# Kernel tuning notes

Hardware: AMD Instinct MI355X
Metric: run time of the kernel (lower is better)

## Reference

```python
import jax, jax.numpy as jnp
import numpy as np

B, C, H, W, E, HEADS = 8, 128, 96, 96, 16, 4
HD = C // HEADS

def _ln(x, g, b, eps=1e-5):
    m = jnp.mean(x, axis=-1, keepdims=True)
    v = jnp.mean(jnp.square(x - m), axis=-1, keepdims=True)
    return (x - m) * jax.lax.rsqrt(v + eps) * g + b

def _gelu(x):
    return jax.nn.gelu(x, approximate=False)  # torch nn.GELU default (erf)

def setup_inputs() -> dict:
    key = jax.random.key(0)
    ks = iter(jax.random.split(key, 48))
    def wgt(shape, s=0.02):
        return jax.random.normal(next(ks), shape, jnp.float32) * s
    d = {
        "feature_map": jax.random.normal(next(ks), (B, C, H, W), jnp.float32),
        "hyperedge_scores": jax.random.uniform(next(ks), (B, H * W, E), jnp.float32),
        # norm_node_pre
        "np_g": jnp.ones((C,), jnp.float32), "np_b": jnp.zeros((C,), jnp.float32),
        # MultiheadAttention (self-attn over hyperedges)
        "mha_w_in": wgt((3 * C, C)), "mha_b_in": jnp.zeros((3 * C,), jnp.float32),
        "mha_w_out": wgt((C, C)), "mha_b_out": jnp.zeros((C,), jnp.float32),
        # transformer FFN
        "ffn_w1": wgt((2 * C, C)), "ffn_b1": jnp.zeros((2 * C,), jnp.float32),
        "ffn_w2": wgt((C, 2 * C)), "ffn_b2": jnp.zeros((C,), jnp.float32),
        # shared LayerNorm inside HypergraphTransformerConv (used twice)
        "tnorm_g": jnp.ones((C,), jnp.float32), "tnorm_b": jnp.zeros((C,), jnp.float32),
        # norm_hyper
        "nh_g": jnp.ones((C,), jnp.float32), "nh_b": jnp.zeros((C,), jnp.float32),
        # hyper_proj
        "hp_w": wgt((C, C)), "hp_b": jnp.zeros((C,), jnp.float32),
        # HyperedgeGuidedNodeAttention
        "q_w": wgt((C, C)), "q_b": jnp.zeros((C,), jnp.float32),
        "kv_w": wgt((2 * C, C)), "kv_b": jnp.zeros((2 * C,), jnp.float32),
        # norm_fusion
        "nf_g": jnp.ones((2 * C,), jnp.float32), "nf_b": jnp.zeros((2 * C,), jnp.float32),
        # gate = Linear(2C->C) + LayerNorm(C) + Sigmoid
        "gate_w": wgt((C, 2 * C)), "gate_b": jnp.zeros((C,), jnp.float32),
        "gate_ln_g": jnp.ones((C,), jnp.float32), "gate_ln_b": jnp.zeros((C,), jnp.float32),
        # node_proj
        "nproj_w": wgt((C, C)), "nproj_b": jnp.zeros((C,), jnp.float32),
    }
    return d

def _forward(feature_map, hyperedge_scores, np_g, np_b, mha_w_in, mha_b_in,
             mha_w_out, mha_b_out, ffn_w1, ffn_b1, ffn_w2, ffn_b2,
             tnorm_g, tnorm_b, nh_g, nh_b, hp_w, hp_b, q_w, q_b, kv_w, kv_b,
             nf_g, nf_b, gate_w, gate_b, gate_ln_g, gate_ln_b, nproj_w, nproj_b):
    b, c, h, w = feature_map.shape
    n = h * w
    node = jnp.transpose(feature_map.reshape(b, c, n), (0, 2, 1))   # [B,N,C]
    node = _ln(node, np_g, np_b)
    # hyperedge aggregation: H^T @ X -> [B,E,C]
    hyper = jnp.einsum('bne,bnc->bec', hyperedge_scores, node)
    # --- HypergraphTransformerConv (self-attn over E=16 hyperedges) ---
    qkv = hyper @ mha_w_in.T + mha_b_in                               # [B,E,3C]
    q, k, v = jnp.split(qkv, 3, axis=-1)
    def heads(x):  # [B,E,C] -> [B,h,E,hd]
        return jnp.transpose(x.reshape(b, E, HEADS, HD), (0, 2, 1, 3))
    q, k, v = heads(q), heads(k), heads(v)
    attn = jax.nn.softmax(jnp.einsum('bhqd,bhkd->bhqk', q, k) / np.sqrt(HD), axis=-1)
    ao = jnp.einsum('bhqk,bhkd->bhqd', attn, v)
    ao = jnp.transpose(ao, (0, 2, 1, 3)).reshape(b, E, c)
    ao = ao @ mha_w_out.T + mha_b_out
    x = _ln(hyper + ao, tnorm_g, tnorm_b)
    ffn = _gelu(x @ ffn_w1.T + ffn_b1) @ ffn_w2.T + ffn_b2
    hyper = _ln(x + ffn, tnorm_g, tnorm_b)
    # ---
    hyper = _ln(hyper, nh_g, nh_b)
    hyper = _gelu(hyper @ hp_w.T + hp_b)                              # [B,E,C]
    intra = jnp.einsum('bne,bec->bnc', hyperedge_scores, hyper)       # [B,N,C]
    # HyperedgeGuidedNodeAttention (scale = C**-0.5)
    Q = node @ q_w.T + q_b
    K, V = jnp.split(hyper @ kv_w.T + kv_b, 2, axis=-1)
    a = jax.nn.softmax(jnp.einsum('bnc,bec->bne', Q, K) * (c ** -0.5), axis=-1)
    cross = jnp.einsum('bne,bec->bnc', a, V)
    combined = _ln(jnp.concatenate([intra, cross], axis=-1), nf_g, nf_b)
    gate = jax.nn.sigmoid(_ln(combined @ gate_w.T + gate_b, gate_ln_g, gate_ln_b))
    fused = gate * intra + (1.0 - gate) * cross
    upd = node + fused                                                # dropout in eval mode
    out = _gelu(upd @ nproj_w.T + nproj_b)
    return jnp.transpose(out, (0, 2, 1)).reshape(b, c, h, w)

def reference(feature_map, hyperedge_scores, np_g, np_b, mha_w_in, mha_b_in,
              mha_w_out, mha_b_out, ffn_w1, ffn_b1, ffn_w2, ffn_b2,
              tnorm_g, tnorm_b, nh_g, nh_b, hp_w, hp_b, q_w, q_b, kv_w, kv_b,
              nf_g, nf_b, gate_w, gate_b, gate_ln_g, gate_ln_b, nproj_w, nproj_b):
    return _forward(feature_map, hyperedge_scores, np_g, np_b, mha_w_in, mha_b_in,
                    mha_w_out, mha_b_out, ffn_w1, ffn_b1, ffn_w2, ffn_b2,
                    tnorm_g, tnorm_b, nh_g, nh_b, hp_w, hp_b, q_w, q_b, kv_w, kv_b,
                    nf_g, nf_b, gate_w, gate_b, gate_ln_g, gate_ln_b, nproj_w, nproj_b)
```

## Files before the change

kernel.cpp:

```cpp
#include <hip/hip_runtime.h>

typedef unsigned short bf_t;
typedef unsigned int u32;
typedef short short8 __attribute__((ext_vector_type(8)));
typedef float f32x4 __attribute__((ext_vector_type(4)));

#define NB 8
#define CC 128
#define NN 9216
#define EE 16

__device__ __forceinline__ float b2f(bf_t u){ return __uint_as_float(((u32)u)<<16); }
__device__ __forceinline__ bf_t f2b(float f){
  u32 u = __float_as_uint(f);
  u = (u + 0x7fffu + ((u>>16)&1u)) >> 16;
  return (bf_t)u;
}
__device__ __forceinline__ u32 pk2(float a, float b){
  return (u32)f2b(a) | ((u32)f2b(b)<<16);
}
__device__ __forceinline__ float gelu_f(float x){ return 0.5f*x*(1.f+erff(x*0.70710678118654752f)); }
__device__ __forceinline__ float red16(float v){
  #pragma unroll
  for (int m=1;m<16;m<<=1) v += __shfl_xor(v, m, 16);
  return v;
}
__device__ __forceinline__ float grs(float var){
  return rsqrtf(fmaxf(var + 1e-5f, 1e-8f));
}
__device__ __forceinline__ short8 ldw8(const float* __restrict__ p){
  float4 a = *(const float4*)p;
  float4 b = *(const float4*)(p+4);
  short8 o;
  o[0]=(short)f2b(a.x); o[1]=(short)f2b(a.y); o[2]=(short)f2b(a.z); o[3]=(short)f2b(a.w);
  o[4]=(short)f2b(b.x); o[5]=(short)f2b(b.y); o[6]=(short)f2b(b.z); o[7]=(short)f2b(b.w);
  return o;
}

__global__ __launch_bounds__(256) void k_zero(float* p){
  int i = blockIdx.x*256 + threadIdx.x;
  if (i < NB*EE*CC) p[i] = 0.f;
}

__global__ __launch_bounds__(256) void k_cvtw(const float* __restrict__ gw,
                                              const float* __restrict__ npw,
                                              bf_t* __restrict__ gwb,
                                              bf_t* __restrict__ npwb){
  int i = blockIdx.x*256 + threadIdx.x;
  gwb[i]        = f2b(gw[i]);
  gwb[i+16384]  = f2b(gw[i+16384]);
  npwb[i]       = f2b(npw[i]);
}

__global__ __launch_bounds__(256) void k_ln_agg(const float* __restrict__ fm,
                                                const float* __restrict__ g,
                                                const float* __restrict__ bb,
                                                const float* __restrict__ sc,
                                                float* __restrict__ nln,
                                                float* __restrict__ hacc){
  int b = blockIdx.y, tid = threadIdx.x;
  __shared__ float xs[128*65];
  __shared__ float scs[64][17];
  __shared__ float ps[4][64], pq[4][64], mrs[2][64];
  int cp = tid&63, eh = tid>>6;
  float a0[4]={0,0,0,0}, a1[4]={0,0,0,0};
  for (int ts=0; ts<4; ts++){
    int n0 = (blockIdx.x*4 + ts)*64;
    const float* base = fm + (size_t)b*CC*NN + n0;
    #pragma unroll
    for (int p=0;p<8;p++){
      int idx = tid + p*256;
      int c = idx>>4, n4 = (idx&15)*4;
      float4 v = *(const float4*)(base + (size_t)c*NN + n4);
      xs[c*65 + n4+0] = v.x; xs[c*65 + n4+1] = v.y;
      xs[c*65 + n4+2] = v.z; xs[c*65 + n4+3] = v.w;
    }
    { int n = tid>>2, e4 = (tid&3)*4;
      float4 sv = *(const float4*)(sc + ((size_t)(b*NN + n0 + n))*EE + e4);
      scs[n][e4+0] = sv.x; scs[n][e4+1] = sv.y;
      scs[n][e4+2] = sv.z; scs[n][e4+3] = sv.w;
    }
    __syncthreads();
    { int cg = tid>>6, n = tid&63;
      float s=0.f, q=0.f;
      #pragma unroll
      for (int c=0;c<32;c++){ float v = xs[(cg*32+c)*65 + n]; s+=v; q+=v*v; }
      ps[cg][n]=s; pq[cg][n]=q;
    }
    __syncthreads();
    if (tid < 64){
      float S = ps[0][tid]+ps[1][tid]+ps[2][tid]+ps[3][tid];
      float Q = pq[0][tid]+pq[1][tid]+pq[2][tid]+pq[3][tid];
      float m = S*(1.f/128.f);
      mrs[0][tid] = m; mrs[1][tid] = grs(Q*(1.f/128.f) - m*m);
    }
    __syncthreads();
    #pragma unroll
    for (int p=0;p<8;p++){
      int idx = tid + p*256;
      int c = idx>>4, n4 = (idx&15)*4;
      float gv = g[c], bv = bb[c];
      float4 o;
      float v0 = (xs[c*65+n4+0]-mrs[0][n4+0])*mrs[1][n4+0]*gv + bv;
      float v1 = (xs[c*65+n4+1]-mrs[0][n4+1])*mrs[1][n4+1]*gv + bv;
      float v2 = (xs[c*65+n4+2]-mrs[0][n4+2])*mrs[1][n4+2]*gv + bv;
      float v3 = (xs[c*65+n4+3]-mrs[0][n4+3])*mrs[1][n4+3]*gv + bv;
      o.x=v0; o.y=v1; o.z=v2; o.w=v3;
      xs[c*65+n4+0]=v0; xs[c*65+n4+1]=v1; xs[c*65+n4+2]=v2; xs[c*65+n4+3]=v3;
      *(float4*)(nln + ((size_t)(b*CC + c))*NN + n0 + n4) = o;
    }
    __syncthreads();
    for (int n=0;n<64;n++){
      float x0 = xs[cp*65 + n], x1 = xs[(cp+64)*65 + n];
      #pragma unroll
      for (int j=0;j<4;j++){
        float se = scs[n][eh*4+j];
        a0[j] += se*x0; a1[j] += se*x1;
      }
    }
    __syncthreads();
  }
  #pragma unroll
  for (int j=0;j<4;j++){
    float* hb = hacc + (size_t)(b*EE + eh*4 + j)*CC;
    atomicAdd(hb + cp, a0[j]);
    atomicAdd(hb + cp + 64, a1[j]);
  }
}

__device__ __forceinline__ void gemm16(const bf_t* A, int SA,
                                       const float* __restrict__ W,
                                       const float* __restrict__ bias,
                                       bf_t* O, int SO, int Nout, int K,
                                       int act, int tid){
  int lane = tid&63, wid = tid>>6;
  int m16 = lane&15, quad = lane>>4;
  for (int n0 = wid*16; n0 < Nout; n0 += 64){
    f32x4 acc = {0.f,0.f,0.f,0.f};
    for (int k0=0;k0<K;k0+=32){
      short8 af = *(const short8*)(A + m16*SA + k0 + quad*8);
      short8 bfv = ldw8(W + (size_t)(n0+m16)*K + k0 + quad*8);
      acc = __builtin_amdgcn_mfma_f32_16x16x32_bf16(af, bfv, acc, 0, 0, 0);
    }
    int col = n0 + m16;
    float bv = bias[col];
    #pragma unroll
    for (int r=0;r<4;r++){
      float v = acc[r] + bv;
      if (act) v = gelu_f(v);
      O[(quad*4+r)*SO + col] = f2b(v);
    }
  }
}

#define SP1 136
#define SP2 264
#define SP3 392

__global__ __launch_bounds__(256) void k_edge(const float* __restrict__ hacc,
    const float* w_in, const float* b_in, const float* w_out, const float* b_out,
    const float* w1, const float* b1, const float* w2, const float* b2v,
    const float* tg, const float* tb, const float* nhg, const float* nhb,
    const float* hpw, const float* hpb, const float* kvw, const float* kvbias,
    const float* qw, const float* qb,
    bf_t* __restrict__ hfw, bf_t* __restrict__ vws,
    float* __restrict__ Ktg, float* __restrict__ qbK){
  __shared__ __align__(16) bf_t hyp0[16*SP1];
  __shared__ __align__(16) bf_t qkvb[16*SP3];
  __shared__ __align__(16) bf_t aob [16*SP1];
  __shared__ __align__(16) bf_t xnb [16*SP1];
  __shared__ __align__(16) bf_t h1b [16*SP2];
  __shared__ __align__(16) bf_t t2b [16*SP1];
  __shared__ __align__(16) bf_t hfb [16*SP1];
  __shared__ __align__(16) bf_t kvo [16*SP2];
  int b = blockIdx.x, tid = threadIdx.x;

  #pragma unroll
  for (int p=0;p<8;p++){
    int idx = tid + p*256;
    int e = idx>>7, c = idx&127;
    hyp0[e*SP1 + c] = f2b(hacc[(size_t)(b*EE + e)*CC + c]);
  }
  __syncthreads();
  gemm16(hyp0, SP1, w_in, b_in, qkvb, SP3, 384, 128, 0, tid);
  __syncthreads();
  {
    int part = tid&3, hq = tid>>2;
    int h = hq>>4, qi = hq&15;
    int dbase = h*32 + part*8;
    float qv[8];
    #pragma unroll
    for (int j=0;j<8;j++) qv[j] = b2f(qkvb[qi*SP3 + dbase + j]);
    float dot[16];
    #pragma unroll
    for (int kk=0;kk<16;kk++){
      float s = 0.f;
      #pragma unroll
      for (int j=0;j<8;j++) s += qv[j]*b2f(qkvb[kk*SP3 + 128 + dbase + j]);
      dot[kk] = s;
    }
    #pragma unroll
    for (int m=1;m<4;m<<=1){
      #pragma unroll
      for (int kk=0;kk<16;kk++) dot[kk] += __shfl_xor(dot[kk], m, 4);
    }
    const float sc1 = 0.17677669529663687f;
    float mx = -1e30f;
    #pragma unroll
    for (int kk=0;kk<16;kk++){ dot[kk] *= sc1; mx = fmaxf(mx, dot[kk]); }
    float sum = 0.f;
    #pragma unroll
    for (int kk=0;kk<16;kk++){ dot[kk] = __expf(dot[kk]-mx); sum += dot[kk]; }
    float inv = 1.f/sum;
    float ao[8] = {0,0,0,0,0,0,0,0};
    #pragma unroll
    for (int kk=0;kk<16;kk++){
      float p = dot[kk]*inv;
      #pragma unroll
      for (int j=0;j<8;j++) ao[j] += p*b2f(qkvb[kk*SP3 + 256 + dbase + j]);
    }
    #pragma unroll
    for (int j=0;j<8;j++) aob[qi*SP1 + dbase + j] = f2b(ao[j]);
  }
  __syncthreads();
  gemm16(aob, SP1, w_out, b_out, xnb, SP1, 128, 128, 0, tid);
  __syncthreads();
  {
    int e = tid>>4, i = tid&15;
    float v[8]; float s=0.f, q=0.f;
    #pragma unroll
    for (int j=0;j<8;j++){
      int c = i*8+j;
      v[j] = b2f(hyp0[e*SP1+c]) + b2f(xnb[e*SP1+c]);
      s += v[j]; q += v[j]*v[j];
    }
    s = red16(s); q = red16(q);
    float m = s*(1.f/128.f);
    float rs = grs(q*(1.f/128.f) - m*m);
    #pragma unroll
    for (int j=0;j<8;j++){
      int c = i*8+j;
      xnb[e*SP1+c] = f2b((v[j]-m)*rs*tg[c] + tb[c]);
    }
  }
  __syncthreads();
  gemm16(xnb, SP1, w1, b1, h1b, SP2, 256, 128, 1, tid);
  __syncthreads();
  gemm16(h1b, SP2, w2, b2v, aob, SP1, 128, 256, 0, tid);
  __syncthreads();
  {
    int e = tid>>4, i = tid&15;
    float v[8]; float s=0.f, q=0.f;
    #pragma unroll
    for (int j=0;j<8;j++){
      int c = i*8+j;
      v[j] = b2f(xnb[e*SP1+c]) + b2f(aob[e*SP1+c]);
      s += v[j]; q += v[j]*v[j];
    }
    s = red16(s); q = red16(q);
    float m = s*(1.f/128.f);
    float rs = grs(q*(1.f/128.f) - m*m);
    float s2=0.f, q2=0.f;
    #pragma unroll
    for (int j=0;j<8;j++){
      int c = i*8+j;
      v[j] = (v[j]-m)*rs*tg[c] + tb[c];
      s2 += v[j]; q2 += v[j]*v[j];
    }
    s2 = red16(s2); q2 = red16(q2);
    float m2 = s2*(1.f/128.f);
    float rs2 = grs(q2*(1.f/128.f) - m2*m2);
    #pragma unroll
    for (int j=0;j<8;j++){
      int c = i*8+j;
      t2b[e*SP1+c] = f2b((v[j]-m2)*rs2*nhg[c] + nhb[c]);
    }
  }
  __syncthreads();
  gemm16(t2b, SP1, hpw, hpb, hfb, SP1, 128, 128, 1, tid);
  __syncthreads();
  gemm16(hfb, SP1, kvw, kvbias, kvo, SP2, 256, 128, 0, tid);
  __syncthreads();
  #pragma unroll
  for (int p=0;p<8;p++){
    int idx = tid + p*256;
    int e = idx>>7, c = idx&127;
    size_t o = (size_t)(b*EE + e)*CC + c;
    hfw[o] = hfb[e*SP1 + c];
    vws[o] = kvo[e*SP2 + 128 + c];
  }
  #pragma unroll
  for (int p=0;p<8;p++){
    int idx = tid + p*256;
    int e = idx>>7, c = idx&127;
    float s = 0.f;
    for (int d=0; d<128; d++) s += b2f(kvo[e*SP2 + d]) * qw[d*128 + c];
    Ktg[(size_t)(b*EE + e)*CC + c] = s;
  }
  if (tid < 16){
    float s = 0.f;
    for (int d=0; d<128; d++) s += qb[d] * b2f(kvo[tid*SP2 + d]);
    qbK[b*EE + tid] = s;
  }
}

template<int PRE>
__global__ __launch_bounds__(256) void k_meganode(
    float* __restrict__ io, const float* __restrict__ sc,
    const bf_t* __restrict__ hf, const bf_t* __restrict__ vw,
    const float* __restrict__ Ktg, const float* __restrict__ qbK,
    const float* __restrict__ nfg, const float* __restrict__ nfb,
    const float* __restrict__ gw, const bf_t* __restrict__ gwb,
    const float* __restrict__ gb,
    const float* __restrict__ glng, const float* __restrict__ glnb,
    const float* __restrict__ npw, const bf_t* __restrict__ npwb,
    const float* __restrict__ npb){
  int tid = threadIdx.x, lane = tid&63, wid = tid>>6;
  int m16 = lane&15, quad = lane>>4;
  int b = blockIdx.y, n0 = blockIdx.x*64;
  __shared__ __align__(16) bf_t xt[64*136];
  __shared__ __align__(16) char ctbuf[34816];
  __shared__ __align__(16) bf_t ktT[16*136];
  __shared__ __align__(16) bf_t hfT[128*24];
  __shared__ __align__(16) bf_t vfT[128*24];
  __shared__ __align__(16) bf_t a_sh[64*24];
  __shared__ float prm[1040];
  bf_t* ct = (bf_t*)ctbuf;
  float* ot = (float*)ctbuf;
  const short8 z8 = {0,0,0,0,0,0,0,0};

  #pragma unroll
  for (int p=0;p<8;p++){
    int idx = tid + p*256;
    int c = idx>>4, n4 = (idx&15)*4;
    float4 v = *(const float4*)(io + ((size_t)(b*CC + c))*NN + n0 + n4);
    xt[(n4+0)*136 + c] = f2b(v.x);
    xt[(n4+1)*136 + c] = f2b(v.y);
    xt[(n4+2)*136 + c] = f2b(v.z);
    xt[(n4+3)*136 + c] = f2b(v.w);
  }
  #pragma unroll
  for (int p=0;p<2;p++){
    int idx = tid + p*256;
    int e = idx>>5, c4 = (idx&31)*4;
    float4 v = *(const float4*)(Ktg + (size_t)(b*EE + e)*CC + c4);
    *(u32*)&ktT[e*136 + c4]     = pk2(v.x, v.y);
    *(u32*)&ktT[e*136 + c4 + 2] = pk2(v.z, v.w);
  }
  { const u32* hs = (const u32*)(hf + (size_t)b*EE*CC);
    const u32* vs = (const u32*)(vw + (size_t)b*EE*CC);
    #pragma unroll
    for (int p=0;p<4;p++){
      int idx = tid + p*256;
      int e = idx>>6, c2 = (idx&63)*2;
      u32 hv = hs[idx], vv = vs[idx];
      hfT[(c2+0)*24 + e] = (bf_t)(hv&0xffffu);
      hfT[(c2+1)*24 + e] = (bf_t)(hv>>16);
      vfT[(c2+0)*24 + e] = (bf_t)(vv&0xffffu);
      vfT[(c2+1)*24 + e] = (bf_t)(vv>>16);
    }
  }
  if (tid < 256){ prm[tid] = nfg[tid]; prm[256+tid] = nfb[tid]; }
  if (tid < 128){ prm[512+tid] = gb[tid]; prm[640+tid] = glng[tid];
                  prm[768+tid] = glnb[tid]; prm[896+tid] = npb[tid]; }
  if (tid < 16) prm[1024+tid] = qbK[b*EE + tid];
  __syncthreads();

  f32x4 dacc = {0.f,0.f,0.f,0.f};
  #pragma unroll
  for (int kk=0;kk<4;kk++){
    short8 a = *(const short8*)(xt + (wid*16+m16)*136 + kk*32 + quad*8);
    short8 bfr = *(const short8*)(ktT + m16*136 + kk*32 + quad*8);
    dacc = __builtin_amdgcn_mfma_f32_16x16x32_bf16(a, bfr, dacc, 0, 0, 0);
  }
  { float qbe = prm[1024 + m16];
    #pragma unroll
    for (int r=0;r<4;r++){
      float v = (dacc[r] + qbe) * 0.08838834764831845f;
      float m = v;
      #pragma unroll
      for (int msk=1;msk<16;msk<<=1) m = fmaxf(m, __shfl_xor(m, msk, 16));
      float ex = __expf(v - m);
      float s = ex;
      #pragma unroll
      for (int msk=1;msk<16;msk<<=1) s += __shfl_xor(s, msk, 16);
      a_sh[(wid*16 + quad*4 + r)*24 + m16] = f2b(ex / s);
    }
  }

  short8 scf = z8, asf = z8;
  if (quad < 2){
    float4 u0 = *(const float4*)(sc + ((size_t)(b*NN + n0 + wid*16 + m16))*EE + quad*8);
    float4 u1 = *(const float4*)(sc + ((size_t)(b*NN + n0 + wid*16 + m16))*EE + quad*8 + 4);
    scf[0]=(short)f2b(u0.x); scf[1]=(short)f2b(u0.y); scf[2]=(short)f2b(u0.z); scf[3]=(short)f2b(u0.w);
    scf[4]=(short)f2b(u1.x); scf[5]=(short)f2b(u1.y); scf[6]=(short)f2b(u1.z); scf[7]=(short)f2b(u1.w);
    asf = *(const short8*)(a_sh + (wid*16+m16)*24 + quad*8);
  }
  f32x4 acc_it[8], acc_cr[8];
  #pragma unroll
  for (int t=0;t<8;t++){
    short8 bh = z8, bv = z8;
    if (quad < 2){
      bh = *(const short8*)(hfT + (t*16+m16)*24 + quad*8);
      bv = *(const short8*)(vfT + (t*16+m16)*24 + quad*8);
    }
    f32x4 zf = {0.f,0.f,0.f,0.f};
    acc_it[t] = __builtin_amdgcn_mfma_f32_16x16x32_bf16(scf, bh, zf, 0, 0, 0);
    acc_cr[t] = __builtin_amdgcn_mfma_f32_16x16x32_bf16(asf, bv, zf, 0, 0, 0);
  }

  { float s4[4]={0,0,0,0}, q4[4]={0,0,0,0};
    #pragma unroll
    for (int t=0;t<8;t++)
      #pragma unroll
      for (int r=0;r<4;r++){
        float a = acc_it[t][r], c = acc_cr[t][r];
        s4[r] += a + c; q4[r] += a*a + c*c;
      }
    #pragma unroll
    for (int r=0;r<4;r++){ s4[r] = red16(s4[r]); q4[r] = red16(q4[r]); }
    #pragma unroll
    for (int r=0;r<4;r++){
      float mean = s4[r]*(1.f/256.f);
      float rstd = grs(q4[r]*(1.f/256.f) - mean*mean);
      int node = wid*16 + quad*4 + r;
      #pragma unroll
      for (int t=0;t<8;t++){
        int ch = t*16 + m16;
        ct[node*272 + ch]       = f2b((acc_it[t][r]-mean)*rstd*prm[ch]     + prm[256+ch]);
        ct[node*272 + 128 + ch] = f2b((acc_cr[t][r]-mean)*rstd*prm[128+ch] + prm[384+ch]);
      }
    }
  }

  short8 af[8];
  #pragma unroll
  for (int kk=0;kk<8;kk++)
    af[kk] = *(const short8*)(ct + (wid*16+m16)*272 + kk*32 + quad*8);
  f32x4 acc_g[8];
  #pragma unroll
  for (int t=0;t<8;t++){
    f32x4 a = {0.f,0.f,0.f,0.f};
    #pragma unroll
    for (int kk=0;kk<8;kk++){
      short8 w8 = PRE ? *(const short8*)(gwb + (size_t)(t*16+m16)*256 + kk*32 + quad*8)
                      : ldw8(gw + (size_t)(t*16+m16)*256 + kk*32 + quad*8);
      a = __builtin_amdgcn_mfma_f32_16x16x32_bf16(af[kk], w8, a, 0, 0, 0);
    }
    acc_g[t] = a;
  }
  __syncthreads();

  { float s2[4]={0,0,0,0}, q2[4]={0,0,0,0};
    #pragma unroll
    for (int t=0;t<8;t++){
      float bv = prm[512 + t*16 + m16];
      #pragma unroll
      for (int r=0;r<4;r++){
        float v = acc_g[t][r] + bv;
        acc_g[t][r] = v; s2[r] += v; q2[r] += v*v;
      }
    }
    #pragma unroll
    for (int r=0;r<4;r++){ s2[r] = red16(s2[r]); q2[r] = red16(q2[r]); }
    #pragma unroll
    for (int t=0;t<8;t++){
      int col = t*16 + m16;
      float lg = prm[640+col], lb = prm[768+col];
      #pragma unroll
      for (int r=0;r<4;r++){
        float m2 = s2[r]*(1.f/128.f);
        float rs2 = grs(q2[r]*(1.f/128.f) - m2*m2);
        float z = (acc_g[t][r]-m2)*rs2*lg + lb;
        float gs = 1.f/(1.f + __expf(-z));
        int node = wid*16 + quad*4 + r;
        float nld = b2f(xt[node*136 + col]);
        xt[node*136 + col] = f2b(nld + gs*acc_it[t][r] + (1.f-gs)*acc_cr[t][r]);
      }
    }
  }

  short8 bfu[4];
  #pragma unroll
  for (int kk=0;kk<4;kk++)
    bfu[kk] = *(const short8*)(xt + (wid*16+m16)*136 + kk*32 + quad*8);
  #pragma unroll
  for (int mt=0;mt<8;mt++){
    f32x4 o = {0.f,0.f,0.f,0.f};
    #pragma unroll
    for (int kk=0;kk<4;kk++){
      short8 aw = PRE ? *(const short8*)(npwb + (size_t)(mt*16+m16)*128 + kk*32 + quad*8)
                      : ldw8(npw + (size_t)(mt*16+m16)*128 + kk*32 + quad*8);
      o = __builtin_amdgcn_mfma_f32_16x16x32_bf16(aw, bfu[kk], o, 0, 0, 0);
    }
    #pragma unroll
    for (int r=0;r<4;r++){
      int cp = mt*16 + quad*4 + r;
      ot[cp*68 + wid*16 + m16] = gelu_f(o[r] + prm[896+cp]);
    }
  }
  __syncthreads();
  #pragma unroll
  for (int p=0;p<8;p++){
    int idx = tid + p*256;
    int c = idx>>4, n4 = (idx&15)*4;
    float4 v = *(const float4*)&ot[c*68 + n4];
    *(float4*)(io + ((size_t)(b*CC + c))*NN + n0 + n4) = v;
  }
}

extern "C" void kernel_launch(void* const* d_in, const int* in_sizes, int n_in,
                              void* d_out, int out_size, void* d_ws, size_t ws_size,
                              hipStream_t stream){
  (void)in_sizes; (void)n_in; (void)out_size;
  const float* fm   = (const float*)d_in[0];
  const float* sc   = (const float*)d_in[1];
  const float* npg  = (const float*)d_in[2];
  const float* npb_ = (const float*)d_in[3];
  const float* w_in = (const float*)d_in[4];
  const float* b_in = (const float*)d_in[5];
  const float* w_out= (const float*)d_in[6];
  const float* b_out= (const float*)d_in[7];
  const float* w1   = (const float*)d_in[8];
  const float* b1   = (const float*)d_in[9];
  const float* w2   = (const float*)d_in[10];
  const float* b2v  = (const float*)d_in[11];
  const float* tg   = (const float*)d_in[12];
  const float* tb   = (const float*)d_in[13];
  const float* nhg  = (const float*)d_in[14];
  const float* nhb  = (const float*)d_in[15];
  const float* hpw  = (const float*)d_in[16];
  const float* hpb  = (const float*)d_in[17];
  const float* qw   = (const float*)d_in[18];
  const float* qb   = (const float*)d_in[19];
  const float* kvw  = (const float*)d_in[20];
  const float* kvb  = (const float*)d_in[21];
  const float* nfg  = (const float*)d_in[22];
  const float* nfb  = (const float*)d_in[23];
  const float* gw   = (const float*)d_in[24];
  const float* gb   = (const float*)d_in[25];
  const float* glng = (const float*)d_in[26];
  const float* glnb = (const float*)d_in[27];
  const float* npw  = (const float*)d_in[28];
  const float* npb2 = (const float*)d_in[29];

  float* nln = (float*)d_out;

  char* w = (char*)d_ws;
  float* hacc = (float*)(w);
  float* Ktg  = (float*)(w + 65536);
  float* qbK  = (float*)(w + 131072);
  bf_t*  hfw  = (bf_t*) (w + 131584);
  bf_t*  vws  = (bf_t*) (w + 164352);
  bf_t*  gwb  = (bf_t*) (w + 197120);
  bf_t*  npwb = (bf_t*) (w + 262656);
  bool pre = (ws_size >= (size_t)295424);

  k_zero  <<<dim3(64),   dim3(256), 0, stream>>>(hacc);
  k_ln_agg<<<dim3(36,8), dim3(256), 0, stream>>>(fm, npg, npb_, sc, nln, hacc);
  k_edge  <<<dim3(8),    dim3(256), 0, stream>>>(hacc, w_in,b_in,w_out,b_out,
                                                 w1,b1,w2,b2v, tg,tb, nhg,nhb,
                                                 hpw,hpb, kvw,kvb, qw,qb,
                                                 hfw, vws, Ktg, qbK);
  if (pre){
    k_cvtw<<<dim3(64), dim3(256), 0, stream>>>(gw, npw, gwb, npwb);
    k_meganode<1><<<dim3(144,8), dim3(256), 0, stream>>>(nln, sc, hfw, vws, Ktg, qbK,
                                                         nfg, nfb, gw, gwb, gb,
                                                         glng, glnb, npw, npwb, npb2);
  } else {
    k_meganode<0><<<dim3(144,8), dim3(256), 0, stream>>>(nln, sc, hfw, vws, Ktg, qbK,
                                                         nfg, nfb, gw, gwb, gb,
                                                         glng, glnb, npw, npwb, npb2);
  }
}
```

Before: 311.5 us.

## Merge prep kernels, shrink meganode shared memory, MFMA-ize Ktg and split ln_agg grid

Fuses the zeroing and weight-conversion kernels into one launch. The ln_agg kernel now processes a single 64-node tile per block over a 144x8 grid instead of looping over four tiles. In k_edge the K·Wq product is computed with MFMA and stored as bf16, and the qb·K reduction is parallelised with shuffles. k_meganode packs its shared memory into one smaller buffer by reusing the concat buffer in two halves, dropping the param staging array and padding, and adds a launch bound of 3 blocks per SM to raise occupancy. The trade-offs are more atomics in ln_agg and parameters now read from global memory.

```diff
diff --git a/kernel.cpp b/kernel.cpp
--- a/kernel.cpp
+++ b/kernel.cpp
@@ -15,9 +15,6 @@
   u32 u = __float_as_uint(f);
   u = (u + 0x7fffu + ((u>>16)&1u)) >> 16;
   return (bf_t)u;
-}
-__device__ __forceinline__ u32 pk2(float a, float b){
-  return (u32)f2b(a) | ((u32)f2b(b)<<16);
 }
 __device__ __forceinline__ float gelu_f(float x){ return 0.5f*x*(1.f+erff(x*0.70710678118654752f)); }
 __device__ __forceinline__ float red16(float v){
@@ -37,19 +34,19 @@
   return o;
 }
 
-__global__ __launch_bounds__(256) void k_zero(float* p){
+template<int PRE>
+__global__ __launch_bounds__(256) void k_pre(float* __restrict__ hacc,
+                                             const float* __restrict__ gw,
+                                             const float* __restrict__ npw,
+                                             bf_t* __restrict__ gwb,
+                                             bf_t* __restrict__ npwb){
   int i = blockIdx.x*256 + threadIdx.x;
-  if (i < NB*EE*CC) p[i] = 0.f;
-}
-
-__global__ __launch_bounds__(256) void k_cvtw(const float* __restrict__ gw,
-                                              const float* __restrict__ npw,
-                                              bf_t* __restrict__ gwb,
-                                              bf_t* __restrict__ npwb){
-  int i = blockIdx.x*256 + threadIdx.x;
-  gwb[i]        = f2b(gw[i]);
-  gwb[i+16384]  = f2b(gw[i+16384]);
-  npwb[i]       = f2b(npw[i]);
+  hacc[i] = 0.f;
+  if (PRE){
+    gwb[i]       = f2b(gw[i]);
+    gwb[i+16384] = f2b(gw[i+16384]);
+    npwb[i]      = f2b(npw[i]);
+  }
 }
 
 __global__ __launch_bounds__(256) void k_ln_agg(const float* __restrict__ fm,
@@ -58,58 +55,56 @@
                                                 const float* __restrict__ sc,
                                                 float* __restrict__ nln,
                                                 float* __restrict__ hacc){
-  int b = blockIdx.y, tid = threadIdx.x;
+  int b = blockIdx.y, n0 = blockIdx.x*64, tid = threadIdx.x;
   __shared__ float xs[128*65];
   __shared__ float scs[64][17];
   __shared__ float ps[4][64], pq[4][64], mrs[2][64];
-  int cp = tid&63, eh = tid>>6;
-  float a0[4]={0,0,0,0}, a1[4]={0,0,0,0};
-  for (int ts=0; ts<4; ts++){
-    int n0 = (blockIdx.x*4 + ts)*64;
-    const float* base = fm + (size_t)b*CC*NN + n0;
-    #pragma unroll
-    for (int p=0;p<8;p++){
-      int idx = tid + p*256;
-      int c = idx>>4, n4 = (idx&15)*4;
-      float4 v = *(const float4*)(base + (size_t)c*NN + n4);
-      xs[c*65 + n4+0] = v.x; xs[c*65 + n4+1] = v.y;
-      xs[c*65 + n4+2] = v.z; xs[c*65 + n4+3] = v.w;
-    }
-    { int n = tid>>2, e4 = (tid&3)*4;
-      float4 sv = *(const float4*)(sc + ((size_t)(b*NN + n0 + n))*EE + e4);
-      scs[n][e4+0] = sv.x; scs[n][e4+1] = sv.y;
-      scs[n][e4+2] = sv.z; scs[n][e4+3] = sv.w;
-    }
-    __syncthreads();
-    { int cg = tid>>6, n = tid&63;
-      float s=0.f, q=0.f;
-      #pragma unroll
-      for (int c=0;c<32;c++){ float v = xs[(cg*32+c)*65 + n]; s+=v; q+=v*v; }
-      ps[cg][n]=s; pq[cg][n]=q;
-    }
-    __syncthreads();
-    if (tid < 64){
-      float S = ps[0][tid]+ps[1][tid]+ps[2][tid]+ps[3][tid];
-      float Q = pq[0][tid]+pq[1][tid]+pq[2][tid]+pq[3][tid];
-      float m = S*(1.f/128.f);
-      mrs[0][tid] = m; mrs[1][tid] = grs(Q*(1.f/128.f) - m*m);
-    }
-    __syncthreads();
-    #pragma unroll
-    for (int p=0;p<8;p++){
-      int idx = tid + p*256;
-      int c = idx>>4, n4 = (idx&15)*4;
-      float gv = g[c], bv = bb[c];
-      float4 o;
-      float v0 = (xs[c*65+n4+0]-mrs[0][n4+0])*mrs[1][n4+0]*gv + bv;
-      float v1 = (xs[c*65+n4+1]-mrs[0][n4+1])*mrs[1][n4+1]*gv + bv;
-      float v2 = (xs[c*65+n4+2]-mrs[0][n4+2])*mrs[1][n4+2]*gv + bv;
-      float v3 = (xs[c*65+n4+3]-mrs[0][n4+3])*mrs[1][n4+3]*gv + bv;
-      o.x=v0; o.y=v1; o.z=v2; o.w=v3;
-      xs[c*65+n4+0]=v0; xs[c*65+n4+1]=v1; xs[c*65+n4+2]=v2; xs[c*65+n4+3]=v3;
-      *(float4*)(nln + ((size_t)(b*CC + c))*NN + n0 + n4) = o;
-    }
-    __syncthreads();
+  const float* base = fm + (size_t)b*CC*NN + n0;
+  #pragma unroll
+  for (int p=0;p<8;p++){
+    int idx = tid + p*256;
+    int c = idx>>4, n4 = (idx&15)*4;
+    float4 v = *(const float4*)(base + (size_t)c*NN + n4);
+    xs[c*65 + n4+0] = v.x; xs[c*65 + n4+1] = v.y;
+    xs[c*65 + n4+2] = v.z; xs[c*65 + n4+3] = v.w;
+  }
+  { int n = tid>>2, e4 = (tid&3)*4;
+    float4 sv = *(const float4*)(sc + ((size_t)(b*NN + n0 + n))*EE + e4);
+    scs[n][e4+0] = sv.x; scs[n][e4+1] = sv.y;
+    scs[n][e4+2] = sv.z; scs[n][e4+3] = sv.w;
+  }
+  __syncthreads();
+  { int cg = tid>>6, n = tid&63;
+    float s=0.f, q=0.f;
+    #pragma unroll
+    for (int c=0;c<32;c++){ float v = xs[(cg*32+c)*65 + n]; s+=v; q+=v*v; }
+    ps[cg][n]=s; pq[cg][n]=q;
+  }
+  __syncthreads();
+  if (tid < 64){
+    float S = ps[0][tid]+ps[1][tid]+ps[2][tid]+ps[3][tid];
+    float Q = pq[0][tid]+pq[1][tid]+pq[2][tid]+pq[3][tid];
+    float m = S*(1.f/128.f);
+    mrs[0][tid] = m; mrs[1][tid] = grs(Q*(1.f/128.f) - m*m);
+  }
+  __syncthreads();
+  #pragma unroll
+  for (int p=0;p<8;p++){
+    int idx = tid + p*256;
+    int c = idx>>4, n4 = (idx&15)*4;
+    float gv = g[c], bv = bb[c];
+    float4 o;
+    float v0 = (xs[c*65+n4+0]-mrs[0][n4+0])*mrs[1][n4+0]*gv + bv;
+    float v1 = (xs[c*65+n4+1]-mrs[0][n4+1])*mrs[1][n4+1]*gv + bv;
+    float v2 = (xs[c*65+n4+2]-mrs[0][n4+2])*mrs[1][n4+2]*gv + bv;
+    float v3 = (xs[c*65+n4+3]-mrs[0][n4+3])*mrs[1][n4+3]*gv + bv;
+    o.x=v0; o.y=v1; o.z=v2; o.w=v3;
+    xs[c*65+n4+0]=v0; xs[c*65+n4+1]=v1; xs[c*65+n4+2]=v2; xs[c*65+n4+3]=v3;
+    *(float4*)(nln + ((size_t)(b*CC + c))*NN + n0 + n4) = o;
+  }
+  __syncthreads();
+  { int cp = tid&63, eh = tid>>6;
+    float a0[4]={0,0,0,0}, a1[4]={0,0,0,0};
     for (int n=0;n<64;n++){
       float x0 = xs[cp*65 + n], x1 = xs[(cp+64)*65 + n];
       #pragma unroll
@@ -118,25 +113,27 @@
         a0[j] += se*x0; a1[j] += se*x1;
       }
     }
-    __syncthreads();
-  }
-  #pragma unroll
-  for (int j=0;j<4;j++){
-    float* hb = hacc + (size_t)(b*EE + eh*4 + j)*CC;
-    atomicAdd(hb + cp, a0[j]);
-    atomicAdd(hb + cp + 64, a1[j]);
-  }
-}
-
+    #pragma unroll
+    for (int j=0;j<4;j++){
+      float* hb = hacc + (size_t)(b*EE + eh*4 + j)*CC;
+      atomicAdd(hb + cp, a0[j]);
+      atomicAdd(hb + cp + 64, a1[j]);
+    }
+  }
+}
+
+template<int K, int NOUT, int ACT>
 __device__ __forceinline__ void gemm16(const bf_t* A, int SA,
                                        const float* __restrict__ W,
                                        const float* __restrict__ bias,
-                                       bf_t* O, int SO, int Nout, int K,
-                                       int act, int tid){
+                                       bf_t* O, int SO, int tid){
   int lane = tid&63, wid = tid>>6;
   int m16 = lane&15, quad = lane>>4;
-  for (int n0 = wid*16; n0 < Nout; n0 += 64){
+  #pragma unroll
+  for (int u=0; u<NOUT/64; u++){
+    int n0 = u*64 + wid*16;
     f32x4 acc = {0.f,0.f,0.f,0.f};
+    #pragma unroll
     for (int k0=0;k0<K;k0+=32){
       short8 af = *(const short8*)(A + m16*SA + k0 + quad*8);
       short8 bfv = ldw8(W + (size_t)(n0+m16)*K + k0 + quad*8);
@@ -147,7 +144,7 @@
     #pragma unroll
     for (int r=0;r<4;r++){
       float v = acc[r] + bv;
-      if (act) v = gelu_f(v);
+      if (ACT) v = gelu_f(v);
       O[(quad*4+r)*SO + col] = f2b(v);
     }
   }
@@ -164,7 +161,7 @@
     const float* hpw, const float* hpb, const float* kvw, const float* kvbias,
     const float* qw, const float* qb,
     bf_t* __restrict__ hfw, bf_t* __restrict__ vws,
-    float* __restrict__ Ktg, float* __restrict__ qbK){
+    bf_t* __restrict__ Ktgb, float* __restrict__ qbK){
   __shared__ __align__(16) bf_t hyp0[16*SP1];
   __shared__ __align__(16) bf_t qkvb[16*SP3];
   __shared__ __align__(16) bf_t aob [16*SP1];
@@ -174,6 +171,7 @@
   __shared__ __align__(16) bf_t hfb [16*SP1];
   __shared__ __align__(16) bf_t kvo [16*SP2];
   int b = blockIdx.x, tid = threadIdx.x;
+  int lane = tid&63, wid = tid>>6, m16 = lane&15, quad = lane>>4;
 
   #pragma unroll
   for (int p=0;p<8;p++){
@@ -182,7 +180,7 @@
     hyp0[e*SP1 + c] = f2b(hacc[(size_t)(b*EE + e)*CC + c]);
   }
   __syncthreads();
-  gemm16(hyp0, SP1, w_in, b_in, qkvb, SP3, 384, 128, 0, tid);
+  gemm16<128,384,0>(hyp0, SP1, w_in, b_in, qkvb, SP3, tid);
   __syncthreads();
   {
     int part = tid&3, hq = tid>>2;
@@ -223,7 +221,7 @@
     for (int j=0;j<8;j++) aob[qi*SP1 + dbase + j] = f2b(ao[j]);
   }
   __syncthreads();
-  gemm16(aob, SP1, w_out, b_out, xnb, SP1, 128, 128, 0, tid);
+  gemm16<128,128,0>(aob, SP1, w_out, b_out, xnb, SP1, tid);
   __syncthreads();
   {
     int e = tid>>4, i = tid&15;
@@ -244,9 +242,9 @@
     }
   }
   __syncthreads();
-  gemm16(xnb, SP1, w1, b1, h1b, SP2, 256, 128, 1, tid);
-  __syncthreads();
-  gemm16(h1b, SP2, w2, b2v, aob, SP1, 128, 256, 0, tid);
+  gemm16<128,256,1>(xnb, SP1, w1, b1, h1b, SP2, tid);
+  __syncthreads();
+  gemm16<256,128,0>(h1b, SP2, w2, b2v, aob, SP1, tid);
   __syncthreads();
   {
     int e = tid>>4, i = tid&15;
@@ -277,9 +275,9 @@
     }
   }
   __syncthreads();
-  gemm16(t2b, SP1, hpw, hpb, hfb, SP1, 128, 128, 1, tid);
-  __syncthreads();
-  gemm16(hfb, SP1, kvw, kvbias, kvo, SP2, 256, 128, 0, tid);
+  gemm16<128,128,1>(t2b, SP1, hpw, hpb, hfb, SP1, tid);
+  __syncthreads();
+  gemm16<128,256,0>(hfb, SP1, kvw, kvbias, kvo, SP2, tid);
   __syncthreads();
   #pragma unroll
   for (int p=0;p<8;p++){
@@ -290,25 +288,36 @@
     vws[o] = kvo[e*SP2 + 128 + c];
   }
   #pragma unroll
-  for (int p=0;p<8;p++){
-    int idx = tid + p*256;
-    int e = idx>>7, c = idx&127;
+  for (int u=0;u<2;u++){
+    int n0 = u*64 + wid*16;
+    f32x4 acc = {0.f,0.f,0.f,0.f};
+    #pragma unroll
+    for (int k0=0;k0<128;k0+=32){
+      short8 a = *(const short8*)(kvo + m16*SP2 + k0 + quad*8);
+      short8 bq;
+      #pragma unroll
+      for (int j=0;j<8;j++)
+        bq[j] = (short)f2b(qw[(size_t)(k0+quad*8+j)*128 + n0+m16]);
+      acc = __builtin_amdgcn_mfma_f32_16x16x32_bf16(a, bq, acc, 0, 0, 0);
+    }
+    #pragma unroll
+    for (int r=0;r<4;r++)
+      Ktgb[(size_t)(b*EE + quad*4 + r)*CC + n0 + m16] = f2b(acc[r]);
+  }
+  { int e = tid>>4, i = tid&15;
     float s = 0.f;
-    for (int d=0; d<128; d++) s += b2f(kvo[e*SP2 + d]) * qw[d*128 + c];
-    Ktg[(size_t)(b*EE + e)*CC + c] = s;
-  }
-  if (tid < 16){
-    float s = 0.f;
-    for (int d=0; d<128; d++) s += qb[d] * b2f(kvo[tid*SP2 + d]);
-    qbK[b*EE + tid] = s;
+    #pragma unroll
+    for (int j=0;j<8;j++) s += qb[i*8+j]*b2f(kvo[e*SP2 + i*8+j]);
+    s = red16(s);
+    if (i == 0) qbK[b*EE + e] = s;
   }
 }
 
 template<int PRE>
-__global__ __launch_bounds__(256) void k_meganode(
+__global__ __launch_bounds__(256,3) void k_meganode(
     float* __restrict__ io, const float* __restrict__ sc,
     const bf_t* __restrict__ hf, const bf_t* __restrict__ vw,
-    const float* __restrict__ Ktg, const float* __restrict__ qbK,
+    const bf_t* __restrict__ ktg, const float* __restrict__ qbK,
     const float* __restrict__ nfg, const float* __restrict__ nfb,
     const float* __restrict__ gw, const bf_t* __restrict__ gwb,
     const float* __restrict__ gb,
@@ -318,15 +327,14 @@
   int tid = threadIdx.x, lane = tid&63, wid = tid>>6;
   int m16 = lane&15, quad = lane>>4;
   int b = blockIdx.y, n0 = blockIdx.x*64;
-  __shared__ __align__(16) bf_t xt[64*136];
-  __shared__ __align__(16) char ctbuf[34816];
-  __shared__ __align__(16) bf_t ktT[16*136];
-  __shared__ __align__(16) bf_t hfT[128*24];
-  __shared__ __align__(16) bf_t vfT[128*24];
-  __shared__ __align__(16) bf_t a_sh[64*24];
-  __shared__ float prm[1040];
-  bf_t* ct = (bf_t*)ctbuf;
-  float* ot = (float*)ctbuf;
+  __shared__ __align__(16) char sm[49408];
+  bf_t* xt  = (bf_t*)(sm);
+  bf_t* ktT = (bf_t*)(sm + 17408);
+  bf_t* ct  = (bf_t*)(sm + 21760);
+  bf_t* hfT = (bf_t*)(sm + 39168);
+  bf_t* vfT = (bf_t*)(sm + 43264);
+  bf_t* ash = (bf_t*)(sm + 47360);
+  float* ot = (float*)(sm);
   const short8 z8 = {0,0,0,0,0,0,0,0};
 
   #pragma unroll
@@ -339,13 +347,13 @@
     xt[(n4+2)*136 + c] = f2b(v.z);
     xt[(n4+3)*136 + c] = f2b(v.w);
   }
-  #pragma unroll
-  for (int p=0;p<2;p++){
-    int idx = tid + p*256;
-    int e = idx>>5, c4 = (idx&31)*4;
-    float4 v = *(const float4*)(Ktg + (size_t)(b*EE + e)*CC + c4);
-    *(u32*)&ktT[e*136 + c4]     = pk2(v.x, v.y);
-    *(u32*)&ktT[e*136 + c4 + 2] = pk2(v.z, v.w);
+  { const u32* kp = (const u32*)(ktg + (size_t)b*EE*CC);
+    #pragma unroll
+    for (int p=0;p<4;p++){
+      int idx = tid + p*256;
+      int e = idx>>6, c2 = (idx&63)*2;
+      *(u32*)&ktT[e*136 + c2] = kp[idx];
+    }
   }
   { const u32* hs = (const u32*)(hf + (size_t)b*EE*CC);
     const u32* vs = (const u32*)(vw + (size_t)b*EE*CC);
@@ -354,16 +362,12 @@
       int idx = tid + p*256;
       int e = idx>>6, c2 = (idx&63)*2;
       u32 hv = hs[idx], vv = vs[idx];
-      hfT[(c2+0)*24 + e] = (bf_t)(hv&0xffffu);
-      hfT[(c2+1)*24 + e] = (bf_t)(hv>>16);
-      vfT[(c2+0)*24 + e] = (bf_t)(vv&0xffffu);
-      vfT[(c2+1)*24 + e] = (bf_t)(vv>>16);
-    }
-  }
-  if (tid < 256){ prm[tid] = nfg[tid]; prm[256+tid] = nfb[tid]; }
-  if (tid < 128){ prm[512+tid] = gb[tid]; prm[640+tid] = glng[tid];
-                  prm[768+tid] = glnb[tid]; prm[896+tid] = npb[tid]; }
-  if (tid < 16) prm[1024+tid] = qbK[b*EE + tid];
+      hfT[(c2+0)*16 + e] = (bf_t)(hv&0xffffu);
+      hfT[(c2+1)*16 + e] = (bf_t)(hv>>16);
+      vfT[(c2+0)*16 + e] = (bf_t)(vv&0xffffu);
+      vfT[(c2+1)*16 + e] = (bf_t)(vv>>16);
+    }
+  }
   __syncthreads();
 
   f32x4 dacc = {0.f,0.f,0.f,0.f};
@@ -373,7 +377,7 @@
     short8 bfr = *(const short8*)(ktT + m16*136 + kk*32 + quad*8);
     dacc = __builtin_amdgcn_mfma_f32_16x16x32_bf16(a, bfr, dacc, 0, 0, 0);
   }
-  { float qbe = prm[1024 + m16];
+  { float qbe = qbK[b*EE + m16];
     #pragma unroll
     for (int r=0;r<4;r++){
       float v = (dacc[r] + qbe) * 0.08838834764831845f;
@@ -384,31 +388,33 @@
       float s = ex;
       #pragma unroll
       for (int msk=1;msk<16;msk<<=1) s += __shfl_xor(s, msk, 16);
-      a_sh[(wid*16 + quad*4 + r)*24 + m16] = f2b(ex / s);
+      ash[(wid*16 + quad*4 + r)*16 + m16] = f2b(ex / s);
     }
   }
 
   short8 scf = z8, asf = z8;
   if (quad < 2){
-    float4 u0 = *(const float4*)(sc + ((size_t)(b*NN + n0 + wid*16 + m16))*EE + quad*8);
-    float4 u1 = *(const float4*)(sc + ((size_t)(b*NN + n0 + wid*16 + m16))*EE + quad*8 + 4);
+    const float* sp = sc + ((size_t)(b*NN + n0 + wid*16 + m16))*EE + quad*8;
+    float4 u0 = *(const float4*)sp;
+    float4 u1 = *(const float4*)(sp+4);
     scf[0]=(short)f2b(u0.x); scf[1]=(short)f2b(u0.y); scf[2]=(short)f2b(u0.z); scf[3]=(short)f2b(u0.w);
     scf[4]=(short)f2b(u1.x); scf[5]=(short)f2b(u1.y); scf[6]=(short)f2b(u1.z); scf[7]=(short)f2b(u1.w);
-    asf = *(const short8*)(a_sh + (wid*16+m16)*24 + quad*8);
+    asf = *(const short8*)(ash + (wid*16+m16)*16 + quad*8);
   }
   f32x4 acc_it[8], acc_cr[8];
   #pragma unroll
   for (int t=0;t<8;t++){
     short8 bh = z8, bv = z8;
     if (quad < 2){
-      bh = *(const short8*)(hfT + (t*16+m16)*24 + quad*8);
-      bv = *(const short8*)(vfT + (t*16+m16)*24 + quad*8);
+      bh = *(const short8*)(hfT + (t*16+m16)*16 + quad*8);
+      bv = *(const short8*)(vfT + (t*16+m16)*16 + quad*8);
     }
     f32x4 zf = {0.f,0.f,0.f,0.f};
     acc_it[t] = __builtin_amdgcn_mfma_f32_16x16x32_bf16(scf, bh, zf, 0, 0, 0);
     acc_cr[t] = __builtin_amdgcn_mfma_f32_16x16x32_bf16(asf, bv, zf, 0, 0, 0);
   }
 
+  float mean4[4], rstd4[4];
   { float s4[4]={0,0,0,0}, q4[4]={0,0,0,0};
     #pragma unroll
     for (int t=0;t<8;t++)
@@ -418,25 +424,38 @@
         s4[r] += a + c; q4[r] += a*a + c*c;
       }
     #pragma unroll
-    for (int r=0;r<4;r++){ s4[r] = red16(s4[r]); q4[r] = red16(q4[r]); }
-    #pragma unroll
     for (int r=0;r<4;r++){
-      float mean = s4[r]*(1.f/256.f);
-      float rstd = grs(q4[r]*(1.f/256.f) - mean*mean);
-      int node = wid*16 + quad*4 + r;
-      #pragma unroll
-      for (int t=0;t<8;t++){
-        int ch = t*16 + m16;
-        ct[node*272 + ch]       = f2b((acc_it[t][r]-mean)*rstd*prm[ch]     + prm[256+ch]);
-        ct[node*272 + 128 + ch] = f2b((acc_cr[t][r]-mean)*rstd*prm[128+ch] + prm[384+ch]);
-      }
-    }
-  }
-
+      s4[r] = red16(s4[r]); q4[r] = red16(q4[r]);
+      mean4[r] = s4[r]*(1.f/256.f);
+      rstd4[r] = grs(q4[r]*(1.f/256.f) - mean4[r]*mean4[r]);
+    }
+  }
   short8 af[8];
   #pragma unroll
-  for (int kk=0;kk<8;kk++)
-    af[kk] = *(const short8*)(ct + (wid*16+m16)*272 + kk*32 + quad*8);
+  for (int r=0;r<4;r++){
+    int node = wid*16 + quad*4 + r;
+    #pragma unroll
+    for (int t=0;t<8;t++){
+      int ch = t*16 + m16;
+      ct[node*136 + ch] = f2b((acc_it[t][r]-mean4[r])*rstd4[r]*nfg[ch] + nfb[ch]);
+    }
+  }
+  #pragma unroll
+  for (int kk=0;kk<4;kk++)
+    af[kk] = *(const short8*)(ct + (wid*16+m16)*136 + kk*32 + quad*8);
+  #pragma unroll
+  for (int r=0;r<4;r++){
+    int node = wid*16 + quad*4 + r;
+    #pragma unroll
+    for (int t=0;t<8;t++){
+      int ch = t*16 + m16;
+      ct[node*136 + ch] = f2b((acc_cr[t][r]-mean4[r])*rstd4[r]*nfg[128+ch] + nfb[128+ch]);
+    }
+  }
+  #pragma unroll
+  for (int kk=0;kk<4;kk++)
+    af[4+kk] = *(const short8*)(ct + (wid*16+m16)*136 + kk*32 + quad*8);
+
   f32x4 acc_g[8];
   #pragma unroll
   for (int t=0;t<8;t++){
@@ -449,12 +468,11 @@
     }
     acc_g[t] = a;
   }
-  __syncthreads();
 
   { float s2[4]={0,0,0,0}, q2[4]={0,0,0,0};
     #pragma unroll
     for (int t=0;t<8;t++){
-      float bv = prm[512 + t*16 + m16];
+      float bv = gb[t*16+m16];
       #pragma unroll
       for (int r=0;r<4;r++){
         float v = acc_g[t][r] + bv;
@@ -466,7 +484,7 @@
     #pragma unroll
     for (int t=0;t<8;t++){
       int col = t*16 + m16;
-      float lg = prm[640+col], lb = prm[768+col];
+      float lg = glng[col], lb = glnb[col];
       #pragma unroll
       for (int r=0;r<4;r++){
         float m2 = s2[r]*(1.f/128.f);
@@ -484,6 +502,7 @@
   #pragma unroll
   for (int kk=0;kk<4;kk++)
     bfu[kk] = *(const short8*)(xt + (wid*16+m16)*136 + kk*32 + quad*8);
+  __syncthreads();
   #pragma unroll
   for (int mt=0;mt<8;mt++){
     f32x4 o = {0.f,0.f,0.f,0.f};
@@ -496,7 +515,7 @@
     #pragma unroll
     for (int r=0;r<4;r++){
       int cp = mt*16 + quad*4 + r;
-      ot[cp*68 + wid*16 + m16] = gelu_f(o[r] + prm[896+cp]);
+      ot[cp*68 + wid*16 + m16] = gelu_f(o[r] + npb[cp]);
     }
   }
   __syncthreads();
@@ -548,28 +567,27 @@
 
   char* w = (char*)d_ws;
   float* hacc = (float*)(w);
-  float* Ktg  = (float*)(w + 65536);
-  float* qbK  = (float*)(w + 131072);
-  bf_t*  hfw  = (bf_t*) (w + 131584);
-  bf_t*  vws  = (bf_t*) (w + 164352);
-  bf_t*  gwb  = (bf_t*) (w + 197120);
-  bf_t*  npwb = (bf_t*) (w + 262656);
-  bool pre = (ws_size >= (size_t)295424);
-
-  k_zero  <<<dim3(64),   dim3(256), 0, stream>>>(hacc);
-  k_ln_agg<<<dim3(36,8), dim3(256), 0, stream>>>(fm, npg, npb_, sc, nln, hacc);
-  k_edge  <<<dim3(8),    dim3(256), 0, stream>>>(hacc, w_in,b_in,w_out,b_out,
-                                                 w1,b1,w2,b2v, tg,tb, nhg,nhb,
-                                                 hpw,hpb, kvw,kvb, qw,qb,
-                                                 hfw, vws, Ktg, qbK);
-  if (pre){
-    k_cvtw<<<dim3(64), dim3(256), 0, stream>>>(gw, npw, gwb, npwb);
-    k_meganode<1><<<dim3(144,8), dim3(256), 0, stream>>>(nln, sc, hfw, vws, Ktg, qbK,
+  float* qbK  = (float*)(w + 65536);
+  bf_t*  hfw  = (bf_t*) (w + 66048);
+  bf_t*  vws  = (bf_t*) (w + 98816);
+  bf_t*  Ktgb = (bf_t*) (w + 131584);
+  bf_t*  gwb  = (bf_t*) (w + 164352);
+  bf_t*  npwb = (bf_t*) (w + 229888);
+  bool pre = (ws_size >= (size_t)262656);
+
+  if (pre) k_pre<1><<<dim3(64), dim3(256), 0, stream>>>(hacc, gw, npw, gwb, npwb);
+  else     k_pre<0><<<dim3(64), dim3(256), 0, stream>>>(hacc, gw, npw, gwb, npwb);
+  k_ln_agg<<<dim3(144,8), dim3(256), 0, stream>>>(fm, npg, npb_, sc, nln, hacc);
+  k_edge  <<<dim3(8),     dim3(256), 0, stream>>>(hacc, w_in,b_in,w_out,b_out,
+                                                  w1,b1,w2,b2v, tg,tb, nhg,nhb,
+                                                  hpw,hpb, kvw,kvb, qw,qb,
+                                                  hfw, vws, Ktgb, qbK);
+  if (pre)
+    k_meganode<1><<<dim3(144,8), dim3(256), 0, stream>>>(nln, sc, hfw, vws, Ktgb, qbK,
                                                          nfg, nfb, gw, gwb, gb,
                                                          glng, glnb, npw, npwb, npb2);
-  } else {
-    k_meganode<0><<<dim3(144,8), dim3(256), 0, stream>>>(nln, sc, hfw, vws, Ktg, qbK,
+  else
+    k_meganode<0><<<dim3(144,8), dim3(256), 0, stream>>>(nln, sc, hfw, vws, Ktgb, qbK,
                                                          nfg, nfb, gw, gwb, gb,
                                                          glng, glnb, npw, npwb, npb2);
-  }
-}
+}
```

Measured after the change: 299.3 us. 3.9% less time.
